# Performance work log

Hardware: AMD Instinct MI355X
Metric: run time of the kernel (lower is better)

The kernel has to match this reference:

```python
import jax, jax.numpy as jnp
import numpy as np

B, C, H, W = 8, 64, 256, 256
M1, M2 = 32, 32  # kept Fourier modes per corner (n_modes//2)
EPS = 1e-5


def _gn(x):
    # GroupNorm(1, C): normalize over (C, H, W) per sample, biased variance
    mu = jnp.mean(x, axis=(1, 2, 3), keepdims=True)
    var = jnp.var(x, axis=(1, 2, 3), keepdims=True)
    return (x - mu) * jax.lax.rsqrt(var + EPS)


def setup_inputs() -> dict:
    key = jax.random.key(0)
    ks = jax.random.split(key, 12)
    spec_scale = 1.0 / (C * C)
    n = lambda k, shape, s=1.0: jax.random.normal(k, shape, dtype=jnp.float32) * s
    return dict(
        x=n(ks[0], (B, C, H, W)),
        t=n(ks[1], (B, C, 1)),
        w1r=n(ks[2], (C, C, M1, M2), spec_scale),
        w1i=n(ks[3], (C, C, M1, M2), spec_scale),
        w2r=n(ks[4], (C, C, M1, M2), spec_scale),
        w2i=n(ks[5], (C, C, M1, M2), spec_scale),
        norm1_w=jnp.ones((C,), jnp.float32),
        norm1_b=jnp.zeros((C,), jnp.float32),
        mlp_w1=n(ks[6], (C // 2, C), 0.05),
        mlp_b1=jnp.zeros((C // 2,), jnp.float32),
        mlp_w2=n(ks[7], (C, C // 2), 0.05),
        mlp_b2=jnp.zeros((C,), jnp.float32),
        gamma_w=n(ks[8], (C, C), 0.05),
        gamma_b=jnp.ones((C,), jnp.float32),
        beta_w=n(ks[9], (C, C), 0.05),
        beta_b=jnp.zeros((C,), jnp.float32),
    )


def reference(x, t, w1r, w1i, w2r, w2i, norm1_w, norm1_b,
              mlp_w1, mlp_b1, mlp_w2, mlp_b2,
              gamma_w, gamma_b, beta_w, beta_b):
    gelu = lambda v: jax.nn.gelu(v, approximate=False)  # torch exact gelu
    skip1 = x
    skip2 = gelu(x)

    # --- SpectralConv: rfft2 -> mode-truncated complex contraction -> irfft2 ---
    xf = jnp.fft.rfftn(x, axes=(2, 3))  # (B, C, H, W//2+1) complex
    b1 = jnp.einsum('bixy,ioxy->boxy', xf[:, :, :M1, :M2], w1r + 1j * w1i)
    b2 = jnp.einsum('bixy,ioxy->boxy', xf[:, :, -M1:, :M2], w2r + 1j * w2i)
    of = (jnp.zeros(xf.shape, xf.dtype)
          .at[:, :, :M1, :M2].set(b1)
          .at[:, :, -M1:, :M2].set(b2))
    y = jnp.fft.irfftn(of, s=(H, W), axes=(2, 3)).astype(x.dtype)

    # norm1 (GroupNorm(1,C) affine) + residual, gelu
    y = _gn(y) * norm1_w[None, :, None, None] + norm1_b[None, :, None, None]
    y = gelu(y + skip1)

    # pointwise MLP (Conv1d 1x1 chain == channel matmuls)
    h = gelu(jnp.einsum('oc,bcxy->boxy', mlp_w1, y) + mlp_b1[None, :, None, None])
    y = jnp.einsum('oc,bcxy->boxy', mlp_w2, h) + mlp_b2[None, :, None, None]

    # timeCondIN: FiLM gamma/beta from t via 1x1 Conv1d, non-affine GroupNorm(1,C)
    gamma = (jnp.einsum('oc,bcl->bol', gamma_w, t) + gamma_b[None, :, None])[..., None]
    beta = (jnp.einsum('oc,bcl->bol', beta_w, t) + beta_b[None, :, None])[..., None]
    y = gamma * _gn(y) + beta

    return y + skip2
```

## Files before the change

### kernel.cpp

```cpp
#include <hip/hip_runtime.h>
#include <math.h>

#define NB 8
#define NC 64
#define NH 256
#define NW 256
#define NHW 65536
#define NM 32
#define NPS 4194304
#define GN_EPS 1e-5f
#define OMEGA 0.0245436926061703f

typedef short shortx8 __attribute__((ext_vector_type(8)));
typedef float floatx4 __attribute__((ext_vector_type(4)));

__device__ __forceinline__ float gelu_f(float v) {
    return 0.5f * v * (1.0f + erff(v * 0.7071067811865475f));
}

__device__ __forceinline__ unsigned short f2bf(float f) {
    unsigned u = __builtin_bit_cast(unsigned, f);
    u = (u + 0x7fffu + ((u >> 16) & 1u)) >> 16;
    return (unsigned short)u;
}

__device__ __forceinline__ float bf2f(unsigned short u) {
    return __builtin_bit_cast(float, ((unsigned)u) << 16);
}

__global__ void k0_init(const float* __restrict__ t_in,
                        const float* __restrict__ gamma_w, const float* __restrict__ gamma_b,
                        const float* __restrict__ beta_w, const float* __restrict__ beta_b,
                        float* __restrict__ gn_acc, float* __restrict__ gamma_bc,
                        float* __restrict__ beta_bc) {
    int t = threadIdx.x;
    if (t < 32) gn_acc[t] = 0.f;
    for (int idx = t; idx < NB * NC; idx += 256) {
        int b = idx >> 6, o = idx & 63;
        float g = gamma_b[o], be = beta_b[o];
        for (int c = 0; c < NC; ++c) {
            float tv = t_in[b * NC + c];
            g += gamma_w[o * NC + c] * tv;
            be += beta_w[o * NC + c] * tv;
        }
        gamma_bc[idx] = g;
        beta_bc[idx] = be;
    }
}

__global__ __launch_bounds__(256) void k_tw(unsigned short* __restrict__ t1h,
                                            unsigned short* __restrict__ t1l,
                                            unsigned short* __restrict__ uh,
                                            unsigned short* __restrict__ ul) {
    int idx = blockIdx.x * 256 + threadIdx.x;
    if (idx >= 16384) return;
    {
        int n = idx >> 8, w = idx & 255;
        float ph = OMEGA * (float)(((n & 31) * w) & 255);
        float s, c;
        sincosf(ph, &s, &c);
        float v = (n < 32) ? c : -s;
        unsigned short h = f2bf(v);
        t1h[idx] = h;
        t1l[idx] = f2bf(v - bf2f(h));
    }
    {
        int w = idx >> 6, k = idx & 63;
        int k31 = k & 31;
        float m = (k31 == 0) ? 1.f : 2.f;
        float ph = OMEGA * (float)((k31 * w) & 255);
        float s, c;
        sincosf(ph, &s, &c);
        float v = (k < 32) ? m * c : -m * s;
        unsigned short h = f2bf(v);
        uh[idx] = h;
        ul[idx] = f2bf(v - bf2f(h));
    }
}

__global__ __launch_bounds__(256, 4) void k1_dftw(const float* __restrict__ x,
                                                  const unsigned short* __restrict__ t1h,
                                                  const unsigned short* __restrict__ t1l,
                                                  float* __restrict__ xw_re,
                                                  float* __restrict__ xw_im) {
    __shared__ unsigned short a_h[128 * 72];
    __shared__ unsigned short a_l[128 * 72];
    int blk = blockIdx.x;
    int bc = blk >> 1;
    int h0 = (blk & 1) * 128;
    const float* src = x + (size_t)bc * NHW + (size_t)h0 * NW;
    int t = threadIdx.x;
    int lane = t & 63, wv = t >> 6, lm = lane & 15, lg = lane >> 4;

    floatx4 acc[2][4] = {};
#pragma unroll
    for (int ks = 0; ks < 4; ++ks) {
        if (ks) __syncthreads();
        for (int i = t; i < 2048; i += 256) {
            int r = i >> 4;
            int c4 = (i & 15) << 2;
            float4 v = *(const float4*)&src[(size_t)r * NW + (ks << 6) + c4];
            int off = r * 72 + c4;
            ushort4 h4, l4;
            h4.x = f2bf(v.x); l4.x = f2bf(v.x - bf2f(h4.x));
            h4.y = f2bf(v.y); l4.y = f2bf(v.y - bf2f(h4.y));
            h4.z = f2bf(v.z); l4.z = f2bf(v.z - bf2f(h4.z));
            h4.w = f2bf(v.w); l4.w = f2bf(v.w - bf2f(h4.w));
            *(ushort4*)&a_h[off] = h4;
            *(ushort4*)&a_l[off] = l4;
        }
        __syncthreads();
#pragma unroll
        for (int kk = 0; kk < 2; ++kk) {
            shortx8 ah[2], al[2], bh[4], bl[4];
#pragma unroll
            for (int mt = 0; mt < 2; ++mt) {
                int off = (wv * 32 + mt * 16 + lm) * 72 + kk * 32 + lg * 8;
                ah[mt] = *(const shortx8*)&a_h[off];
                al[mt] = *(const shortx8*)&a_l[off];
            }
#pragma unroll
            for (int nt = 0; nt < 4; ++nt) {
                int off = (nt * 16 + lm) * 256 + ks * 64 + kk * 32 + lg * 8;
                bh[nt] = *(const shortx8*)&t1h[off];
                bl[nt] = *(const shortx8*)&t1l[off];
            }
#pragma unroll
            for (int mt = 0; mt < 2; ++mt)
#pragma unroll
                for (int nt = 0; nt < 4; ++nt) {
                    acc[mt][nt] = __builtin_amdgcn_mfma_f32_16x16x32_bf16(ah[mt], bh[nt], acc[mt][nt], 0, 0, 0);
                    acc[mt][nt] = __builtin_amdgcn_mfma_f32_16x16x32_bf16(ah[mt], bl[nt], acc[mt][nt], 0, 0, 0);
                    acc[mt][nt] = __builtin_amdgcn_mfma_f32_16x16x32_bf16(al[mt], bh[nt], acc[mt][nt], 0, 0, 0);
                }
        }
    }
    size_t rowg = (size_t)bc * NH + h0;
#pragma unroll
    for (int mt = 0; mt < 2; ++mt)
#pragma unroll
        for (int nt = 0; nt < 4; ++nt) {
            int n = nt * 16 + lm;
            float* dst = (n < 32) ? xw_re : xw_im;
            int kx = n & 31;
#pragma unroll
            for (int r = 0; r < 4; ++r) {
                int row = wv * 32 + mt * 16 + lg * 4 + r;
                dst[(rowg + row) * NM + kx] = acc[mt][nt][r];
            }
        }
}

__global__ __launch_bounds__(256) void k2_dfth(const float* __restrict__ xw_re,
                                               const float* __restrict__ xw_im,
                                               float* __restrict__ xf_re,
                                               float* __restrict__ xf_im) {
    __shared__ float xr_l[NH * NM];
    __shared__ float xi_l[NH * NM];
    int bc = blockIdx.x;
    size_t base = (size_t)bc * NH * NM;
    for (int idx = threadIdx.x; idx < NH * NM / 4; idx += 256) {
        ((float4*)xr_l)[idx] = ((const float4*)(xw_re + base))[idx];
        ((float4*)xi_l)[idx] = ((const float4*)(xw_im + base))[idx];
    }
    __syncthreads();
    int t = threadIdx.x;
    int kx = t & 31, jgrp = t >> 5;
    float cd[8], sd[8], cc[8], ss[8], ar[8], ai[8];
#pragma unroll
    for (int jj = 0; jj < 8; ++jj) {
        int j = jgrp * 8 + jj;
        int f = (j < 32) ? j : 192 + j;
        sincosf(OMEGA * (float)f, &sd[jj], &cd[jj]);
        cc[jj] = 1.f; ss[jj] = 0.f; ar[jj] = 0.f; ai[jj] = 0.f;
    }
    for (int h = 0; h < 256; ++h) {
        float xr = xr_l[h * NM + kx], xi = xi_l[h * NM + kx];
#pragma unroll
        for (int jj = 0; jj < 8; ++jj) {
            ar[jj] += xr * cc[jj] + xi * ss[jj];
            ai[jj] += xi * cc[jj] - xr * ss[jj];
            float c2 = cc[jj] * cd[jj] - ss[jj] * sd[jj];
            ss[jj] = ss[jj] * cd[jj] + cc[jj] * sd[jj];
            cc[jj] = c2;
        }
    }
    size_t ob = (size_t)bc * 2048;
#pragma unroll
    for (int jj = 0; jj < 8; ++jj) {
        int j = jgrp * 8 + jj;
        xf_re[ob + j * 32 + kx] = ar[jj];
        xf_im[ob + j * 32 + kx] = ai[jj];
    }
}

__global__ __launch_bounds__(256) void k3_mix(const float* __restrict__ xf_re,
                                              const float* __restrict__ xf_im,
                                              const float* __restrict__ w1r, const float* __restrict__ w1i,
                                              const float* __restrict__ w2r, const float* __restrict__ w2i,
                                              float* __restrict__ yf_re, float* __restrict__ yf_im) {
    __shared__ float xr_l[4 * 64 * 32];
    __shared__ float xi_l[4 * 64 * 32];
    int blk = blockIdx.x;
    int bh = blk & 1;
    int oct = (blk >> 1) & 7;
    int ky = blk >> 4;
    for (int idx = threadIdx.x; idx < 4 * 64 * 32; idx += 256) {
        int bb = idx >> 11;
        int i = (idx >> 5) & 63;
        int kx = idx & 31;
        size_t g = ((size_t)((bh * 4 + bb) * 64 + i) * 64 + ky) * 32 + kx;
        xr_l[idx] = xf_re[g];
        xi_l[idx] = xf_im[g];
    }
    __syncthreads();
    const float* wr = (ky < 32) ? w1r : w2r;
    const float* wi = (ky < 32) ? w1i : w2i;
    int kyl = ky & 31;
    int t = threadIdx.x;
    int kx = t & 31, oo = t >> 5;
    int o = oct * 8 + oo;
    float accr[4] = {0.f, 0.f, 0.f, 0.f};
    float acci[4] = {0.f, 0.f, 0.f, 0.f};
    for (int i = 0; i < 64; ++i) {
        size_t wbase = ((size_t)(i * 64 + o) * 32 + kyl) * 32 + kx;
        float wrv = wr[wbase];
        float wiv = wi[wbase];
#pragma unroll
        for (int bb = 0; bb < 4; ++bb) {
            float xr = xr_l[(bb * 64 + i) * 32 + kx];
            float xi = xi_l[(bb * 64 + i) * 32 + kx];
            accr[bb] += xr * wrv - xi * wiv;
            acci[bb] += xr * wiv + xi * wrv;
        }
    }
#pragma unroll
    for (int bb = 0; bb < 4; ++bb) {
        int b = bh * 4 + bb;
        size_t g = ((size_t)(b * 64 + o) * 64 + ky) * 32 + kx;
        yf_re[g] = accr[bb];
        yf_im[g] = acci[bb];
    }
}

__global__ __launch_bounds__(256) void k4_idfth(const float* __restrict__ yf_re,
                                                const float* __restrict__ yf_im,
                                                float* __restrict__ yh_re,
                                                float* __restrict__ yh_im) {
    __shared__ float yr_l[2048];
    __shared__ float yi_l[2048];
    int blk = blockIdx.x;
    int bc = blk >> 2, hq = blk & 3;
    size_t base = (size_t)bc * 2048;
    for (int idx = threadIdx.x; idx < 512; idx += 256) {
        ((float4*)yr_l)[idx] = ((const float4*)(yf_re + base))[idx];
        ((float4*)yi_l)[idx] = ((const float4*)(yf_im + base))[idx];
    }
    __syncthreads();
    int t = threadIdx.x;
    int kx = t & 31, hgrp = t >> 5;
    int h0 = hq * 64 + hgrp * 8;
    float cdh[8], sdh[8], cc[8], ss[8], ar[8], ai[8];
#pragma unroll
    for (int hh = 0; hh < 8; ++hh) {
        sincosf(OMEGA * (float)(h0 + hh), &sdh[hh], &cdh[hh]);
        cc[hh] = 1.f; ss[hh] = 0.f; ar[hh] = 0.f; ai[hh] = 0.f;
    }
    for (int j = 0; j < 64; ++j) {
        if (j == 32) {
#pragma unroll
            for (int hh = 0; hh < 8; ++hh) ss[hh] = -ss[hh];
        }
        float yr = yr_l[j * 32 + kx], yi = yi_l[j * 32 + kx];
#pragma unroll
        for (int hh = 0; hh < 8; ++hh) {
            ar[hh] += yr * cc[hh] - yi * ss[hh];
            ai[hh] += yr * ss[hh] + yi * cc[hh];
            float c2 = cc[hh] * cdh[hh] - ss[hh] * sdh[hh];
            ss[hh] = ss[hh] * cdh[hh] + cc[hh] * sdh[hh];
            cc[hh] = c2;
        }
    }
    const float sc = 1.0f / 65536.0f;
#pragma unroll
    for (int hh = 0; hh < 8; ++hh) {
        size_t g = ((size_t)bc * NH + h0 + hh) * NM + kx;
        yh_re[g] = ar[hh] * sc;
        yh_im[g] = ai[hh] * sc;
    }
}

__global__ __launch_bounds__(256, 2) void k5_irfftw(const float* __restrict__ yh_re,
                                                    const float* __restrict__ yh_im,
                                                    const unsigned short* __restrict__ uh,
                                                    const unsigned short* __restrict__ ul,
                                                    float* __restrict__ yout,
                                                    float* __restrict__ gn_acc) {
    __shared__ unsigned short a_h[128 * 72];
    __shared__ unsigned short a_l[128 * 72];
    __shared__ float red[8];
    int blk = blockIdx.x;
    size_t row0 = (size_t)blk * 128;
    int t = threadIdx.x;

    for (int i = t; i < 1024; i += 256) {
        int r = i >> 3;
        int c4 = (i & 7) << 2;
        float4 vr = *(const float4*)&yh_re[(row0 + r) * NM + c4];
        float4 vi = *(const float4*)&yh_im[(row0 + r) * NM + c4];
        int offr = r * 72 + c4;
        ushort4 h4, l4;
        h4.x = f2bf(vr.x); l4.x = f2bf(vr.x - bf2f(h4.x));
        h4.y = f2bf(vr.y); l4.y = f2bf(vr.y - bf2f(h4.y));
        h4.z = f2bf(vr.z); l4.z = f2bf(vr.z - bf2f(h4.z));
        h4.w = f2bf(vr.w); l4.w = f2bf(vr.w - bf2f(h4.w));
        *(ushort4*)&a_h[offr] = h4;
        *(ushort4*)&a_l[offr] = l4;
        h4.x = f2bf(vi.x); l4.x = f2bf(vi.x - bf2f(h4.x));
        h4.y = f2bf(vi.y); l4.y = f2bf(vi.y - bf2f(h4.y));
        h4.z = f2bf(vi.z); l4.z = f2bf(vi.z - bf2f(h4.z));
        h4.w = f2bf(vi.w); l4.w = f2bf(vi.w - bf2f(h4.w));
        *(ushort4*)&a_h[offr + 32] = h4;
        *(ushort4*)&a_l[offr + 32] = l4;
    }
    __syncthreads();

    int lane = t & 63, wv = t >> 6, lm = lane & 15, lg = lane >> 4;
    floatx4 acc[2][16] = {};
#pragma unroll
    for (int kk = 0; kk < 2; ++kk) {
        shortx8 ah[2], al[2];
#pragma unroll
        for (int mt = 0; mt < 2; ++mt) {
            int off = (wv * 32 + mt * 16 + lm) * 72 + kk * 32 + lg * 8;
            ah[mt] = *(const shortx8*)&a_h[off];
            al[mt] = *(const shortx8*)&a_l[off];
        }
#pragma unroll
        for (int nt = 0; nt < 16; ++nt) {
            int w = nt * 16 + lm;
            shortx8 bh = *(const shortx8*)&uh[w * 64 + kk * 32 + lg * 8];
            shortx8 bl = *(const shortx8*)&ul[w * 64 + kk * 32 + lg * 8];
#pragma unroll
            for (int mt = 0; mt < 2; ++mt) {
                acc[mt][nt] = __builtin_amdgcn_mfma_f32_16x16x32_bf16(ah[mt], bh, acc[mt][nt], 0, 0, 0);
                acc[mt][nt] = __builtin_amdgcn_mfma_f32_16x16x32_bf16(ah[mt], bl, acc[mt][nt], 0, 0, 0);
                acc[mt][nt] = __builtin_amdgcn_mfma_f32_16x16x32_bf16(al[mt], bh, acc[mt][nt], 0, 0, 0);
            }
        }
    }

    float sum = 0.f, sq = 0.f;
#pragma unroll
    for (int mt = 0; mt < 2; ++mt)
#pragma unroll
        for (int nt = 0; nt < 16; ++nt) {
            int w = nt * 16 + lm;
#pragma unroll
            for (int r = 0; r < 4; ++r) {
                int row = wv * 32 + mt * 16 + lg * 4 + r;
                float v = acc[mt][nt][r];
                yout[(row0 + row) * NW + w] = v;
                sum += v;
                sq += v * v;
            }
        }
#pragma unroll
    for (int off = 32; off > 0; off >>= 1) {
        sum += __shfl_down(sum, off);
        sq += __shfl_down(sq, off);
    }
    if (lane == 0) { red[wv] = sum; red[4 + wv] = sq; }
    __syncthreads();
    if (t == 0) {
        int b = blk >> 7;
        atomicAdd(&gn_acc[b * 4 + 0], red[0] + red[1] + red[2] + red[3]);
        atomicAdd(&gn_acc[b * 4 + 1], red[4] + red[5] + red[6] + red[7]);
    }
}

__global__ __launch_bounds__(256, 2) void k6_mlp(const float* __restrict__ x,
                                                 const float* __restrict__ norm1_w,
                                                 const float* __restrict__ norm1_b,
                                                 const float* __restrict__ mlp_w1,
                                                 const float* __restrict__ mlp_b1,
                                                 const float* __restrict__ mlp_w2,
                                                 const float* __restrict__ mlp_b2,
                                                 float* __restrict__ y,
                                                 float* __restrict__ gn_acc) {
    __shared__ __align__(16) unsigned char smem[77728];
    unsigned short* vbuf_h = (unsigned short*)smem;
    unsigned short* vbuf_l = (unsigned short*)(smem + 18432);
    unsigned short* w1_h   = (unsigned short*)(smem + 36864);
    unsigned short* w1_l   = (unsigned short*)(smem + 41472);
    unsigned short* hbuf_h = (unsigned short*)(smem + 46080);
    unsigned short* hbuf_l = (unsigned short*)(smem + 56320);
    unsigned short* w2_h   = (unsigned short*)(smem + 66560);
    unsigned short* w2_l   = (unsigned short*)(smem + 71680);
    float* outbuf = (float*)smem;
    float* nwl = (float*)(smem + 76800);
    float* nbl = nwl + 64;
    float* b1l = nbl + 64;
    float* b2l = b1l + 32;
    float* red = b2l + 64;

    int t = threadIdx.x;
    int blk = blockIdx.x;
    int b = blk >> 9;
    int pixbase = (blk & 511) * 128;
    size_t bbase = (size_t)b * NC * NHW + pixbase;

    if (t < 64) { nwl[t] = norm1_w[t]; nbl[t] = norm1_b[t]; b2l[t] = mlp_b2[t]; }
    if (t >= 64 && t < 96) b1l[t - 64] = mlp_b1[t - 64];
    for (int idx = t; idx < 2048; idx += 256) {
        float wv1 = mlp_w1[idx];
        unsigned short h1 = f2bf(wv1);
        int r1 = (idx >> 6) * 72 + (idx & 63);
        w1_h[r1] = h1;
        w1_l[r1] = f2bf(wv1 - bf2f(h1));
        float wv2 = mlp_w2[idx];
        unsigned short h2 = f2bf(wv2);
        int r2 = (idx >> 5) * 40 + (idx & 31);
        w2_h[r2] = h2;
        w2_l[r2] = f2bf(wv2 - bf2f(h2));
    }
    __syncthreads();

    const float invN = 1.0f / (float)NPS;
    float m1 = gn_acc[b * 4 + 0] * invN;
    float var1 = gn_acc[b * 4 + 1] * invN - m1 * m1;
    float rs1 = rsqrtf(var1 + GN_EPS);
    {
        int p = t & 127;
        int c0 = (t >> 7) * 32;
        size_t base = bbase + (size_t)c0 * NHW + p;
#pragma unroll 8
        for (int ci = 0; ci < 32; ++ci) {
            float yv = y[base + (size_t)ci * NHW];
            float xv = x[base + (size_t)ci * NHW];
            int c = c0 + ci;
            float g = (yv - m1) * rs1 * nwl[c] + nbl[c] + xv;
            float vv = gelu_f(g);
            unsigned short vh = f2bf(vv);
            vbuf_h[p * 72 + c] = vh;
            vbuf_l[p * 72 + c] = f2bf(vv - bf2f(vh));
        }
    }
    __syncthreads();

    int lane = t & 63, wv = t >> 6;
    int lm = lane & 15, lg = lane >> 4;

    floatx4 acc1[2][2] = {};
#pragma unroll
    for (int ks = 0; ks < 2; ++ks) {
        shortx8 ah[2], al[2], bh[2], bl[2];
#pragma unroll
        for (int mt = 0; mt < 2; ++mt) {
            int off = (wv * 32 + mt * 16 + lm) * 72 + lg * 8 + ks * 32;
            ah[mt] = *(const shortx8*)&vbuf_h[off];
            al[mt] = *(const shortx8*)&vbuf_l[off];
        }
#pragma unroll
        for (int nt = 0; nt < 2; ++nt) {
            int off = (nt * 16 + lm) * 72 + lg * 8 + ks * 32;
            bh[nt] = *(const shortx8*)&w1_h[off];
            bl[nt] = *(const shortx8*)&w1_l[off];
        }
#pragma unroll
        for (int mt = 0; mt < 2; ++mt)
#pragma unroll
            for (int nt = 0; nt < 2; ++nt) {
                acc1[mt][nt] = __builtin_amdgcn_mfma_f32_16x16x32_bf16(ah[mt], bh[nt], acc1[mt][nt], 0, 0, 0);
                acc1[mt][nt] = __builtin_amdgcn_mfma_f32_16x16x32_bf16(ah[mt], bl[nt], acc1[mt][nt], 0, 0, 0);
                acc1[mt][nt] = __builtin_amdgcn_mfma_f32_16x16x32_bf16(al[mt], bh[nt], acc1[mt][nt], 0, 0, 0);
            }
    }
#pragma unroll
    for (int mt = 0; mt < 2; ++mt)
#pragma unroll
        for (int nt = 0; nt < 2; ++nt) {
            float b1v = b1l[nt * 16 + lm];
#pragma unroll
            for (int r = 0; r < 4; ++r) {
                float hv = gelu_f(acc1[mt][nt][r] + b1v);
                unsigned short hh = f2bf(hv);
                int off = (wv * 32 + mt * 16 + lg * 4 + r) * 40 + nt * 16 + lm;
                hbuf_h[off] = hh;
                hbuf_l[off] = f2bf(hv - bf2f(hh));
            }
        }
    __syncthreads();

    floatx4 acc2[2][4] = {};
    {
        shortx8 ah2[2], al2[2], bh2[4], bl2[4];
#pragma unroll
        for (int mt = 0; mt < 2; ++mt) {
            int off = (wv * 32 + mt * 16 + lm) * 40 + lg * 8;
            ah2[mt] = *(const shortx8*)&hbuf_h[off];
            al2[mt] = *(const shortx8*)&hbuf_l[off];
        }
#pragma unroll
        for (int nt = 0; nt < 4; ++nt) {
            int off = (nt * 16 + lm) * 40 + lg * 8;
            bh2[nt] = *(const shortx8*)&w2_h[off];
            bl2[nt] = *(const shortx8*)&w2_l[off];
        }
#pragma unroll
        for (int mt = 0; mt < 2; ++mt)
#pragma unroll
            for (int nt = 0; nt < 4; ++nt) {
                acc2[mt][nt] = __builtin_amdgcn_mfma_f32_16x16x32_bf16(ah2[mt], bh2[nt], acc2[mt][nt], 0, 0, 0);
                acc2[mt][nt] = __builtin_amdgcn_mfma_f32_16x16x32_bf16(ah2[mt], bl2[nt], acc2[mt][nt], 0, 0, 0);
                acc2[mt][nt] = __builtin_amdgcn_mfma_f32_16x16x32_bf16(al2[mt], bh2[nt], acc2[mt][nt], 0, 0, 0);
            }
    }
    __syncthreads();

#pragma unroll
    for (int mt = 0; mt < 2; ++mt)
#pragma unroll
        for (int nt = 0; nt < 4; ++nt) {
            int ch = nt * 16 + lm;
            float b2v = b2l[ch];
#pragma unroll
            for (int r = 0; r < 4; ++r)
                outbuf[ch * 132 + wv * 32 + mt * 16 + lg * 4 + r] = acc2[mt][nt][r] + b2v;
        }
    __syncthreads();

    float sum = 0.f, sq = 0.f;
#pragma unroll
    for (int it = 0; it < 8; ++it) {
        int flat = it * 256 + t;
        int c = flat >> 5;
        int p4 = (flat & 31) * 4;
        float4 v = *(const float4*)&outbuf[c * 132 + p4];
        *(float4*)&y[bbase + (size_t)c * NHW + p4] = v;
        sum += v.x + v.y + v.z + v.w;
        sq += v.x * v.x + v.y * v.y + v.z * v.z + v.w * v.w;
    }
#pragma unroll
    for (int off = 32; off > 0; off >>= 1) {
        sum += __shfl_down(sum, off);
        sq += __shfl_down(sq, off);
    }
    if (lane == 0) { red[wv] = sum; red[4 + wv] = sq; }
    __syncthreads();
    if (t == 0) {
        atomicAdd(&gn_acc[b * 4 + 2], red[0] + red[1] + red[2] + red[3]);
        atomicAdd(&gn_acc[b * 4 + 3], red[4] + red[5] + red[6] + red[7]);
    }
}

__global__ __launch_bounds__(256) void k7_final(const float* __restrict__ x,
                                                const float* __restrict__ gamma_bc,
                                                const float* __restrict__ beta_bc,
                                                const float* __restrict__ gn_acc,
                                                float* __restrict__ y) {
    size_t idx4 = (size_t)blockIdx.x * 256 + threadIdx.x;
    size_t base = idx4 * 4;
    int b = (int)(base >> 22);
    int c = (int)((base >> 16) & 63);
    const float invN = 1.0f / (float)NPS;
    float m2 = gn_acc[b * 4 + 2] * invN;
    float var2 = gn_acc[b * 4 + 3] * invN - m2 * m2;
    float rs2 = rsqrtf(var2 + GN_EPS);
    float g = gamma_bc[b * 64 + c];
    float be = beta_bc[b * 64 + c];
    float4 yv = ((float4*)y)[idx4];
    float4 xv = ((const float4*)x)[idx4];
    yv.x = g * ((yv.x - m2) * rs2) + be + gelu_f(xv.x);
    yv.y = g * ((yv.y - m2) * rs2) + be + gelu_f(xv.y);
    yv.z = g * ((yv.z - m2) * rs2) + be + gelu_f(xv.z);
    yv.w = g * ((yv.w - m2) * rs2) + be + gelu_f(xv.w);
    ((float4*)y)[idx4] = yv;
}

extern "C" void kernel_launch(void* const* d_in, const int* in_sizes, int n_in,
                              void* d_out, int out_size, void* d_ws, size_t ws_size,
                              hipStream_t stream) {
    (void)in_sizes; (void)n_in; (void)out_size; (void)ws_size;
    const float* x       = (const float*)d_in[0];
    const float* t_in    = (const float*)d_in[1];
    const float* w1r     = (const float*)d_in[2];
    const float* w1i     = (const float*)d_in[3];
    const float* w2r     = (const float*)d_in[4];
    const float* w2i     = (const float*)d_in[5];
    const float* norm1_w = (const float*)d_in[6];
    const float* norm1_b = (const float*)d_in[7];
    const float* mlp_w1  = (const float*)d_in[8];
    const float* mlp_b1  = (const float*)d_in[9];
    const float* mlp_w2  = (const float*)d_in[10];
    const float* mlp_b2  = (const float*)d_in[11];
    const float* gamma_w = (const float*)d_in[12];
    const float* gamma_b = (const float*)d_in[13];
    const float* beta_w  = (const float*)d_in[14];
    const float* beta_b  = (const float*)d_in[15];
    float* out = (float*)d_out;
    float* ws  = (float*)d_ws;

    float* gn_acc   = ws;
    float* gamma_bc = ws + 32;
    float* beta_bc  = ws + 544;
    float* xw_re    = ws + 2048;
    float* xw_im    = xw_re + 4194304;
    float* xf_re    = xw_im + 4194304;
    float* xf_im    = xf_re + 1048576;
    float* yf_re    = xf_im + 1048576;
    float* yf_im    = yf_re + 1048576;
    unsigned short* t1h = (unsigned short*)(yf_im + 1048576);
    unsigned short* t1l = t1h + 16384;
    unsigned short* uh  = t1l + 16384;
    unsigned short* ul  = uh + 16384;

    k_tw<<<dim3(64), dim3(256), 0, stream>>>(t1h, t1l, uh, ul);
    k0_init<<<dim3(1), dim3(256), 0, stream>>>(t_in, gamma_w, gamma_b, beta_w, beta_b,
                                               gn_acc, gamma_bc, beta_bc);
    k1_dftw<<<dim3(1024), dim3(256), 0, stream>>>(x, t1h, t1l, xw_re, xw_im);
    k2_dfth<<<dim3(512), dim3(256), 0, stream>>>(xw_re, xw_im, xf_re, xf_im);
    k3_mix<<<dim3(1024), dim3(256), 0, stream>>>(xf_re, xf_im, w1r, w1i, w2r, w2i,
                                                 yf_re, yf_im);
    k4_idfth<<<dim3(2048), dim3(256), 0, stream>>>(yf_re, yf_im, xw_re, xw_im);
    k5_irfftw<<<dim3(1024), dim3(256), 0, stream>>>(xw_re, xw_im, uh, ul, out, gn_acc);
    k6_mlp<<<dim3(4096), dim3(256), 0, stream>>>(x, norm1_w, norm1_b, mlp_w1, mlp_b1,
                                                 mlp_w2, mlp_b2, out, gn_acc);
    k7_final<<<dim3(32768), dim3(256), 0, stream>>>(x, gamma_bc, beta_bc, gn_acc, out);
}
```

Measured before the change: 727.3 us.

## Move H-direction DFTs onto bf16x3 MFMA with precomputed twiddle matrices

Recasts the forward and inverse H-axis DFT stages (k2, k4) as matrix multiplies against precomputed bf16 hi/lo twiddle matrices, using split-bf16 MFMA in place of scalar recurrence loops. It also moves the MLP weight bf16 splitting into the init kernel so every k6 block copies pre-split weights, and vectorizes k6's input staging with float4 loads. The aim is to cut ALU-bound DFT time and per-block redundant conversion. In exchange the twiddle kernel does more work and uses extra workspace, and the three-term bf16 split may give slightly different precision than the fp32 recurrence.

```diff
diff --git a/kernel.cpp b/kernel.cpp
--- a/kernel.cpp
+++ b/kernel.cpp
@@ -31,8 +31,11 @@
 __global__ void k0_init(const float* __restrict__ t_in,
                         const float* __restrict__ gamma_w, const float* __restrict__ gamma_b,
                         const float* __restrict__ beta_w, const float* __restrict__ beta_b,
+                        const float* __restrict__ mlp_w1, const float* __restrict__ mlp_w2,
                         float* __restrict__ gn_acc, float* __restrict__ gamma_bc,
-                        float* __restrict__ beta_bc) {
+                        float* __restrict__ beta_bc,
+                        unsigned short* __restrict__ w1p_h, unsigned short* __restrict__ w1p_l,
+                        unsigned short* __restrict__ w2p_h, unsigned short* __restrict__ w2p_l) {
     int t = threadIdx.x;
     if (t < 32) gn_acc[t] = 0.f;
     for (int idx = t; idx < NB * NC; idx += 256) {
@@ -46,15 +49,28 @@
         gamma_bc[idx] = g;
         beta_bc[idx] = be;
     }
+    for (int idx = t; idx < 2048; idx += 256) {
+        float wv1 = mlp_w1[idx];
+        unsigned short h1 = f2bf(wv1);
+        w1p_h[idx] = h1;
+        w1p_l[idx] = f2bf(wv1 - bf2f(h1));
+        float wv2 = mlp_w2[idx];
+        unsigned short h2 = f2bf(wv2);
+        w2p_h[idx] = h2;
+        w2p_l[idx] = f2bf(wv2 - bf2f(h2));
+    }
 }
 
 __global__ __launch_bounds__(256) void k_tw(unsigned short* __restrict__ t1h,
                                             unsigned short* __restrict__ t1l,
                                             unsigned short* __restrict__ uh,
-                                            unsigned short* __restrict__ ul) {
+                                            unsigned short* __restrict__ ul,
+                                            unsigned short* __restrict__ m2h,
+                                            unsigned short* __restrict__ m2l,
+                                            unsigned short* __restrict__ m4h,
+                                            unsigned short* __restrict__ m4l) {
     int idx = blockIdx.x * 256 + threadIdx.x;
-    if (idx >= 16384) return;
-    {
+    if (idx < 16384) {
         int n = idx >> 8, w = idx & 255;
         float ph = OMEGA * (float)(((n & 31) * w) & 255);
         float s, c;
@@ -63,18 +79,41 @@
         unsigned short h = f2bf(v);
         t1h[idx] = h;
         t1l[idx] = f2bf(v - bf2f(h));
-    }
-    {
-        int w = idx >> 6, k = idx & 63;
+
+        int w2 = idx >> 6, k = idx & 63;
         int k31 = k & 31;
         float m = (k31 == 0) ? 1.f : 2.f;
-        float ph = OMEGA * (float)((k31 * w) & 255);
+        float ph2 = OMEGA * (float)((k31 * w2) & 255);
+        sincosf(ph2, &s, &c);
+        float v2 = (k < 32) ? m * c : -m * s;
+        h = f2bf(v2);
+        uh[idx] = h;
+        ul[idx] = f2bf(v2 - bf2f(h));
+    }
+    {
+        int m = idx >> 9, k = idx & 511;
+        int j = m & 63;
+        int f = (j < 32) ? j : 192 + j;
+        int h256 = k & 255;
         float s, c;
-        sincosf(ph, &s, &c);
-        float v = (k < 32) ? m * c : -m * s;
-        unsigned short h = f2bf(v);
-        uh[idx] = h;
-        ul[idx] = f2bf(v - bf2f(h));
+        sincosf(OMEGA * (float)((f * h256) & 255), &s, &c);
+        float v = (m < 64) ? ((k < 256) ? c : s) : ((k < 256) ? -s : c);
+        unsigned short hh = f2bf(v);
+        m2h[idx] = hh;
+        m2l[idx] = f2bf(v - bf2f(hh));
+    }
+    {
+        const float sc = 1.0f / 65536.0f;
+        int m = idx >> 7, k = idx & 127;
+        int h256 = m & 255;
+        int j = k & 63;
+        int f = (j < 32) ? j : 192 + j;
+        float s, c;
+        sincosf(OMEGA * (float)((f * h256) & 255), &s, &c);
+        float v = ((m < 256) ? ((k < 64) ? c : -s) : ((k < 64) ? s : c)) * sc;
+        unsigned short hh = f2bf(v);
+        m4h[idx] = hh;
+        m4l[idx] = f2bf(v - bf2f(hh));
     }
 }
 
@@ -151,47 +190,76 @@
         }
 }
 
-__global__ __launch_bounds__(256) void k2_dfth(const float* __restrict__ xw_re,
-                                               const float* __restrict__ xw_im,
-                                               float* __restrict__ xf_re,
-                                               float* __restrict__ xf_im) {
-    __shared__ float xr_l[NH * NM];
-    __shared__ float xi_l[NH * NM];
+__global__ __launch_bounds__(256, 2) void k2_dfth(const float* __restrict__ xw_re,
+                                                  const float* __restrict__ xw_im,
+                                                  const unsigned short* __restrict__ m2h,
+                                                  const unsigned short* __restrict__ m2l,
+                                                  float* __restrict__ xf_re,
+                                                  float* __restrict__ xf_im) {
+    __shared__ unsigned short bt_h[32 * 520];
+    __shared__ unsigned short bt_l[32 * 520];
     int bc = blockIdx.x;
-    size_t base = (size_t)bc * NH * NM;
-    for (int idx = threadIdx.x; idx < NH * NM / 4; idx += 256) {
-        ((float4*)xr_l)[idx] = ((const float4*)(xw_re + base))[idx];
-        ((float4*)xi_l)[idx] = ((const float4*)(xw_im + base))[idx];
-    }
-    __syncthreads();
+    size_t base = (size_t)bc * (NH * NM);
     int t = threadIdx.x;
-    int kx = t & 31, jgrp = t >> 5;
-    float cd[8], sd[8], cc[8], ss[8], ar[8], ai[8];
-#pragma unroll
-    for (int jj = 0; jj < 8; ++jj) {
-        int j = jgrp * 8 + jj;
-        int f = (j < 32) ? j : 192 + j;
-        sincosf(OMEGA * (float)f, &sd[jj], &cd[jj]);
-        cc[jj] = 1.f; ss[jj] = 0.f; ar[jj] = 0.f; ai[jj] = 0.f;
-    }
-    for (int h = 0; h < 256; ++h) {
-        float xr = xr_l[h * NM + kx], xi = xi_l[h * NM + kx];
-#pragma unroll
-        for (int jj = 0; jj < 8; ++jj) {
-            ar[jj] += xr * cc[jj] + xi * ss[jj];
-            ai[jj] += xi * cc[jj] - xr * ss[jj];
-            float c2 = cc[jj] * cd[jj] - ss[jj] * sd[jj];
-            ss[jj] = ss[jj] * cd[jj] + cc[jj] * sd[jj];
-            cc[jj] = c2;
-        }
+    for (int idx4 = t; idx4 < 2048; idx4 += 256) {
+        int h = idx4 >> 3;
+        int kxg = (idx4 & 7) << 2;
+        float4 vr = ((const float4*)(xw_re + base))[idx4];
+        float4 vi = ((const float4*)(xw_im + base))[idx4];
+        float fr[4] = {vr.x, vr.y, vr.z, vr.w};
+        float fi[4] = {vi.x, vi.y, vi.z, vi.w};
+#pragma unroll
+        for (int q = 0; q < 4; ++q) {
+            int rowo = (kxg + q) * 520;
+            unsigned short hh = f2bf(fr[q]);
+            bt_h[rowo + h] = hh;
+            bt_l[rowo + h] = f2bf(fr[q] - bf2f(hh));
+            hh = f2bf(fi[q]);
+            bt_h[rowo + 256 + h] = hh;
+            bt_l[rowo + 256 + h] = f2bf(fi[q] - bf2f(hh));
+        }
+    }
+    __syncthreads();
+
+    int lane = t & 63, wv = t >> 6, lm = lane & 15, lg = lane >> 4;
+    floatx4 acc[2][2] = {};
+#pragma unroll
+    for (int ks = 0; ks < 16; ++ks) {
+        shortx8 bh[2], bl[2], ah[2], al[2];
+#pragma unroll
+        for (int nt = 0; nt < 2; ++nt) {
+            int off = (nt * 16 + lm) * 520 + ks * 32 + lg * 8;
+            bh[nt] = *(const shortx8*)&bt_h[off];
+            bl[nt] = *(const shortx8*)&bt_l[off];
+        }
+#pragma unroll
+        for (int mt = 0; mt < 2; ++mt) {
+            int off = (wv * 32 + mt * 16 + lm) * 512 + ks * 32 + lg * 8;
+            ah[mt] = *(const shortx8*)&m2h[off];
+            al[mt] = *(const shortx8*)&m2l[off];
+        }
+#pragma unroll
+        for (int mt = 0; mt < 2; ++mt)
+#pragma unroll
+            for (int nt = 0; nt < 2; ++nt) {
+                acc[mt][nt] = __builtin_amdgcn_mfma_f32_16x16x32_bf16(ah[mt], bh[nt], acc[mt][nt], 0, 0, 0);
+                acc[mt][nt] = __builtin_amdgcn_mfma_f32_16x16x32_bf16(ah[mt], bl[nt], acc[mt][nt], 0, 0, 0);
+                acc[mt][nt] = __builtin_amdgcn_mfma_f32_16x16x32_bf16(al[mt], bh[nt], acc[mt][nt], 0, 0, 0);
+            }
     }
     size_t ob = (size_t)bc * 2048;
 #pragma unroll
-    for (int jj = 0; jj < 8; ++jj) {
-        int j = jgrp * 8 + jj;
-        xf_re[ob + j * 32 + kx] = ar[jj];
-        xf_im[ob + j * 32 + kx] = ai[jj];
-    }
+    for (int mt = 0; mt < 2; ++mt)
+#pragma unroll
+        for (int nt = 0; nt < 2; ++nt) {
+            int n = nt * 16 + lm;
+#pragma unroll
+            for (int r = 0; r < 4; ++r) {
+                int row = wv * 32 + mt * 16 + lg * 4 + r;
+                float* dst = (row < 64) ? xf_re : xf_im;
+                dst[ob + (row & 63) * 32 + n] = acc[mt][nt][r];
+            }
+        }
 }
 
 __global__ __launch_bounds__(256) void k3_mix(const float* __restrict__ xf_re,
@@ -243,51 +311,74 @@
     }
 }
 
-__global__ __launch_bounds__(256) void k4_idfth(const float* __restrict__ yf_re,
-                                                const float* __restrict__ yf_im,
-                                                float* __restrict__ yh_re,
-                                                float* __restrict__ yh_im) {
-    __shared__ float yr_l[2048];
-    __shared__ float yi_l[2048];
-    int blk = blockIdx.x;
-    int bc = blk >> 2, hq = blk & 3;
+__global__ __launch_bounds__(256, 2) void k4_idfth(const float* __restrict__ yf_re,
+                                                   const float* __restrict__ yf_im,
+                                                   const unsigned short* __restrict__ m4h,
+                                                   const unsigned short* __restrict__ m4l,
+                                                   float* __restrict__ yh_re,
+                                                   float* __restrict__ yh_im) {
+    __shared__ unsigned short bt_h[32 * 136];
+    __shared__ unsigned short bt_l[32 * 136];
+    int bc = blockIdx.x;
     size_t base = (size_t)bc * 2048;
-    for (int idx = threadIdx.x; idx < 512; idx += 256) {
-        ((float4*)yr_l)[idx] = ((const float4*)(yf_re + base))[idx];
-        ((float4*)yi_l)[idx] = ((const float4*)(yf_im + base))[idx];
-    }
-    __syncthreads();
     int t = threadIdx.x;
-    int kx = t & 31, hgrp = t >> 5;
-    int h0 = hq * 64 + hgrp * 8;
-    float cdh[8], sdh[8], cc[8], ss[8], ar[8], ai[8];
-#pragma unroll
-    for (int hh = 0; hh < 8; ++hh) {
-        sincosf(OMEGA * (float)(h0 + hh), &sdh[hh], &cdh[hh]);
-        cc[hh] = 1.f; ss[hh] = 0.f; ar[hh] = 0.f; ai[hh] = 0.f;
-    }
-    for (int j = 0; j < 64; ++j) {
-        if (j == 32) {
-#pragma unroll
-            for (int hh = 0; hh < 8; ++hh) ss[hh] = -ss[hh];
-        }
-        float yr = yr_l[j * 32 + kx], yi = yi_l[j * 32 + kx];
-#pragma unroll
-        for (int hh = 0; hh < 8; ++hh) {
-            ar[hh] += yr * cc[hh] - yi * ss[hh];
-            ai[hh] += yr * ss[hh] + yi * cc[hh];
-            float c2 = cc[hh] * cdh[hh] - ss[hh] * sdh[hh];
-            ss[hh] = ss[hh] * cdh[hh] + cc[hh] * sdh[hh];
-            cc[hh] = c2;
-        }
-    }
-    const float sc = 1.0f / 65536.0f;
-#pragma unroll
-    for (int hh = 0; hh < 8; ++hh) {
-        size_t g = ((size_t)bc * NH + h0 + hh) * NM + kx;
-        yh_re[g] = ar[hh] * sc;
-        yh_im[g] = ai[hh] * sc;
-    }
+    for (int idx4 = t; idx4 < 512; idx4 += 256) {
+        int j = idx4 >> 3;
+        int kxg = (idx4 & 7) << 2;
+        float4 vr = ((const float4*)(yf_re + base))[idx4];
+        float4 vi = ((const float4*)(yf_im + base))[idx4];
+        float fr[4] = {vr.x, vr.y, vr.z, vr.w};
+        float fi[4] = {vi.x, vi.y, vi.z, vi.w};
+#pragma unroll
+        for (int q = 0; q < 4; ++q) {
+            int rowo = (kxg + q) * 136;
+            unsigned short hh = f2bf(fr[q]);
+            bt_h[rowo + j] = hh;
+            bt_l[rowo + j] = f2bf(fr[q] - bf2f(hh));
+            hh = f2bf(fi[q]);
+            bt_h[rowo + 64 + j] = hh;
+            bt_l[rowo + 64 + j] = f2bf(fi[q] - bf2f(hh));
+        }
+    }
+    __syncthreads();
+
+    int lane = t & 63, wv = t >> 6, lm = lane & 15, lg = lane >> 4;
+    floatx4 acc[8][2] = {};
+#pragma unroll
+    for (int ks = 0; ks < 4; ++ks) {
+        shortx8 bh[2], bl[2];
+#pragma unroll
+        for (int nt = 0; nt < 2; ++nt) {
+            int off = (nt * 16 + lm) * 136 + ks * 32 + lg * 8;
+            bh[nt] = *(const shortx8*)&bt_h[off];
+            bl[nt] = *(const shortx8*)&bt_l[off];
+        }
+#pragma unroll
+        for (int mt = 0; mt < 8; ++mt) {
+            int off = (wv * 128 + mt * 16 + lm) * 128 + ks * 32 + lg * 8;
+            shortx8 ah = *(const shortx8*)&m4h[off];
+            shortx8 al = *(const shortx8*)&m4l[off];
+#pragma unroll
+            for (int nt = 0; nt < 2; ++nt) {
+                acc[mt][nt] = __builtin_amdgcn_mfma_f32_16x16x32_bf16(ah, bh[nt], acc[mt][nt], 0, 0, 0);
+                acc[mt][nt] = __builtin_amdgcn_mfma_f32_16x16x32_bf16(ah, bl[nt], acc[mt][nt], 0, 0, 0);
+                acc[mt][nt] = __builtin_amdgcn_mfma_f32_16x16x32_bf16(al, bh[nt], acc[mt][nt], 0, 0, 0);
+            }
+        }
+    }
+    size_t ob = (size_t)bc * (NH * NM);
+#pragma unroll
+    for (int mt = 0; mt < 8; ++mt)
+#pragma unroll
+        for (int nt = 0; nt < 2; ++nt) {
+            int n = nt * 16 + lm;
+#pragma unroll
+            for (int r = 0; r < 4; ++r) {
+                int row = wv * 128 + mt * 16 + lg * 4 + r;
+                float* dst = (row < 256) ? yh_re : yh_im;
+                dst[ob + (row & 255) * 32 + n] = acc[mt][nt][r];
+            }
+        }
 }
 
 __global__ __launch_bounds__(256, 2) void k5_irfftw(const float* __restrict__ yh_re,
@@ -382,9 +473,11 @@
 __global__ __launch_bounds__(256, 2) void k6_mlp(const float* __restrict__ x,
                                                  const float* __restrict__ norm1_w,
                                                  const float* __restrict__ norm1_b,
-                                                 const float* __restrict__ mlp_w1,
+                                                 const unsigned short* __restrict__ w1p_h,
+                                                 const unsigned short* __restrict__ w1p_l,
+                                                 const unsigned short* __restrict__ w2p_h,
+                                                 const unsigned short* __restrict__ w2p_l,
                                                  const float* __restrict__ mlp_b1,
-                                                 const float* __restrict__ mlp_w2,
                                                  const float* __restrict__ mlp_b2,
                                                  float* __restrict__ y,
                                                  float* __restrict__ gn_acc) {
@@ -412,17 +505,14 @@
 
     if (t < 64) { nwl[t] = norm1_w[t]; nbl[t] = norm1_b[t]; b2l[t] = mlp_b2[t]; }
     if (t >= 64 && t < 96) b1l[t - 64] = mlp_b1[t - 64];
-    for (int idx = t; idx < 2048; idx += 256) {
-        float wv1 = mlp_w1[idx];
-        unsigned short h1 = f2bf(wv1);
-        int r1 = (idx >> 6) * 72 + (idx & 63);
-        w1_h[r1] = h1;
-        w1_l[r1] = f2bf(wv1 - bf2f(h1));
-        float wv2 = mlp_w2[idx];
-        unsigned short h2 = f2bf(wv2);
-        int r2 = (idx >> 5) * 40 + (idx & 31);
-        w2_h[r2] = h2;
-        w2_l[r2] = f2bf(wv2 - bf2f(h2));
+#pragma unroll
+    for (int idx4 = t; idx4 < 512; idx4 += 256) {
+        int r1 = idx4 >> 4, c1 = (idx4 & 15) << 2;
+        *(ushort4*)&w1_h[r1 * 72 + c1] = ((const ushort4*)w1p_h)[idx4];
+        *(ushort4*)&w1_l[r1 * 72 + c1] = ((const ushort4*)w1p_l)[idx4];
+        int r2 = idx4 >> 3, c2 = (idx4 & 7) << 2;
+        *(ushort4*)&w2_h[r2 * 40 + c2] = ((const ushort4*)w2p_h)[idx4];
+        *(ushort4*)&w2_l[r2 * 40 + c2] = ((const ushort4*)w2p_l)[idx4];
     }
     __syncthreads();
 
@@ -431,19 +521,26 @@
     float var1 = gn_acc[b * 4 + 1] * invN - m1 * m1;
     float rs1 = rsqrtf(var1 + GN_EPS);
     {
-        int p = t & 127;
-        int c0 = (t >> 7) * 32;
-        size_t base = bbase + (size_t)c0 * NHW + p;
-#pragma unroll 8
-        for (int ci = 0; ci < 32; ++ci) {
-            float yv = y[base + (size_t)ci * NHW];
-            float xv = x[base + (size_t)ci * NHW];
-            int c = c0 + ci;
-            float g = (yv - m1) * rs1 * nwl[c] + nbl[c] + xv;
-            float vv = gelu_f(g);
-            unsigned short vh = f2bf(vv);
-            vbuf_h[p * 72 + c] = vh;
-            vbuf_l[p * 72 + c] = f2bf(vv - bf2f(vh));
+        int pg = (t & 31) << 2;
+        int cg = (t >> 5) << 3;
+#pragma unroll
+        for (int ci = 0; ci < 8; ++ci) {
+            int c = cg + ci;
+            size_t rb = bbase + (size_t)c * NHW + pg;
+            float4 yv4 = *(const float4*)&y[rb];
+            float4 xv4 = *(const float4*)&x[rb];
+            float nw = nwl[c], nb = nbl[c];
+            float gv[4];
+            gv[0] = gelu_f((yv4.x - m1) * rs1 * nw + nb + xv4.x);
+            gv[1] = gelu_f((yv4.y - m1) * rs1 * nw + nb + xv4.y);
+            gv[2] = gelu_f((yv4.z - m1) * rs1 * nw + nb + xv4.z);
+            gv[3] = gelu_f((yv4.w - m1) * rs1 * nw + nb + xv4.w);
+#pragma unroll
+            for (int q = 0; q < 4; ++q) {
+                unsigned short vh = f2bf(gv[q]);
+                vbuf_h[(pg + q) * 72 + c] = vh;
+                vbuf_l[(pg + q) * 72 + c] = f2bf(gv[q] - bf2f(vh));
+            }
         }
     }
     __syncthreads();
@@ -614,17 +711,28 @@
     unsigned short* t1l = t1h + 16384;
     unsigned short* uh  = t1l + 16384;
     unsigned short* ul  = uh + 16384;
-
-    k_tw<<<dim3(64), dim3(256), 0, stream>>>(t1h, t1l, uh, ul);
+    unsigned short* w1p_h = ul + 16384;
+    unsigned short* w1p_l = w1p_h + 2048;
+    unsigned short* w2p_h = w1p_l + 2048;
+    unsigned short* w2p_l = w2p_h + 2048;
+    unsigned short* m2h = w2p_l + 2048;
+    unsigned short* m2l = m2h + 65536;
+    unsigned short* m4h = m2l + 65536;
+    unsigned short* m4l = m4h + 65536;
+
+    k_tw<<<dim3(256), dim3(256), 0, stream>>>(t1h, t1l, uh, ul, m2h, m2l, m4h, m4l);
     k0_init<<<dim3(1), dim3(256), 0, stream>>>(t_in, gamma_w, gamma_b, beta_w, beta_b,
-                                               gn_acc, gamma_bc, beta_bc);
+                                               mlp_w1, mlp_w2,
+                                               gn_acc, gamma_bc, beta_bc,
+                                               w1p_h, w1p_l, w2p_h, w2p_l);
     k1_dftw<<<dim3(1024), dim3(256), 0, stream>>>(x, t1h, t1l, xw_re, xw_im);
-    k2_dfth<<<dim3(512), dim3(256), 0, stream>>>(xw_re, xw_im, xf_re, xf_im);
+    k2_dfth<<<dim3(512), dim3(256), 0, stream>>>(xw_re, xw_im, m2h, m2l, xf_re, xf_im);
     k3_mix<<<dim3(1024), dim3(256), 0, stream>>>(xf_re, xf_im, w1r, w1i, w2r, w2i,
                                                  yf_re, yf_im);
-    k4_idfth<<<dim3(2048), dim3(256), 0, stream>>>(yf_re, yf_im, xw_re, xw_im);
+    k4_idfth<<<dim3(512), dim3(256), 0, stream>>>(yf_re, yf_im, m4h, m4l, xw_re, xw_im);
     k5_irfftw<<<dim3(1024), dim3(256), 0, stream>>>(xw_re, xw_im, uh, ul, out, gn_acc);
-    k6_mlp<<<dim3(4096), dim3(256), 0, stream>>>(x, norm1_w, norm1_b, mlp_w1, mlp_b1,
-                                                 mlp_w2, mlp_b2, out, gn_acc);
+    k6_mlp<<<dim3(4096), dim3(256), 0, stream>>>(x, norm1_w, norm1_b,
+                                                 w1p_h, w1p_l, w2p_h, w2p_l,
+                                                 mlp_b1, mlp_b2, out, gn_acc);
     k7_final<<<dim3(32768), dim3(256), 0, stream>>>(x, gamma_bc, beta_bc, gn_acc, out);
 }
```

Result: faster. 667.5 us (-8.2%).
